# Kernel optimization log

Measured on AMD Instinct MI355X. Metric: run time of the kernel, lower is better.

Reference implementation:

```python
import jax, jax.numpy as jnp
import numpy as np

B, S, E, H = 4, 1024, 1024, 16
HD = E // H  # head_dim = 64


def setup_inputs() -> dict:
    key = jax.random.key(0)
    ks = jax.random.split(key, 7)
    return {
        "query": jax.random.normal(ks[0], (B, S, E), dtype=jnp.float32),
        "key": jax.random.normal(ks[1], (B, S, E), dtype=jnp.float32),
        "value": jax.random.normal(ks[2], (B, S, E), dtype=jnp.float32),
        # per-head Linear weights stacked: [H, head_dim, emb_dim] (torch Linear is y = x @ W^T)
        "Wq": jax.random.normal(ks[3], (H, HD, E), dtype=jnp.float32) * (E ** -0.5),
        "Wk": jax.random.normal(ks[4], (H, HD, E), dtype=jnp.float32) * (E ** -0.5),
        "Wv": jax.random.normal(ks[5], (H, HD, E), dtype=jnp.float32) * (E ** -0.5),
        "Wo": jax.random.normal(ks[6], (E, E), dtype=jnp.float32) * (E ** -0.5),
    }


def reference(query, key, value, Wq, Wk, Wv, Wo):
    # Project per head (all heads vectorized): [B,S,E] x [H,HD,E] -> [B,H,S,HD]
    Q = jnp.einsum('bse,hde->bhsd', query, Wq)
    K = jnp.einsum('bse,hde->bhsd', key, Wk)
    V = jnp.einsum('bse,hde->bhsd', value, Wv)
    scale = 1.0 / np.sqrt(HD)  # source divides by sqrt(emb_dim / n_head)
    scores = jnp.einsum('bhsd,bhtd->bhst', Q, K) * scale  # [B,H,S,S]
    p = jax.nn.softmax(scores, axis=-1)
    ctx = jnp.einsum('bhst,bhtd->bhsd', p, V)  # [B,H,S,HD]
    # concat heads along feature dim -> [B,S,E]
    concat = ctx.transpose(0, 2, 1, 3).reshape(query.shape[0], query.shape[1], -1)
    return concat @ Wo.T
```

## Files before the change

kernel.cpp:

```cpp
#include <hip/hip_runtime.h>

typedef __bf16 bf16_t;
typedef __bf16 bf16x8 __attribute__((ext_vector_type(8)));
typedef float f32x4 __attribute__((ext_vector_type(4)));

#define E_DIM 1024
#define S_LEN 1024
#define NHEAD 16
#define HD_DIM 64
#define BATCH 4
#define TOKENS 4096

__device__ __forceinline__ void async_copy16(const bf16_t* g, bf16_t* l) {
    __builtin_amdgcn_global_load_lds((const __attribute__((address_space(1))) void*)g,
                                     (__attribute__((address_space(3))) void*)l,
                                     16, 0, 0);
}

__global__ __launch_bounds__(256) void cast3(const float* __restrict__ a,
                                             const float* __restrict__ b,
                                             const float* __restrict__ c,
                                             bf16_t* __restrict__ dst, int n) {
    const float* src = blockIdx.y == 0 ? a : (blockIdx.y == 1 ? b : c);
    dst += (size_t)blockIdx.y * n;
    int i = (blockIdx.x * 256 + threadIdx.x) * 8;
    if (i + 8 > n) return;
    float4 x = *(const float4*)(src + i);
    float4 y = *(const float4*)(src + i + 4);
    bf16x8 o;
    o[0] = (bf16_t)x.x; o[1] = (bf16_t)x.y; o[2] = (bf16_t)x.z; o[3] = (bf16_t)x.w;
    o[4] = (bf16_t)y.x; o[5] = (bf16_t)y.y; o[6] = (bf16_t)y.z; o[7] = (bf16_t)y.w;
    *(bf16x8*)(dst + i) = o;
}

__global__ __launch_bounds__(256) void cast4(const float* __restrict__ a,
                                             const float* __restrict__ b,
                                             const float* __restrict__ c,
                                             const float* __restrict__ d,
                                             bf16_t* __restrict__ dst, int n) {
    const float* src = blockIdx.y == 0 ? a : (blockIdx.y == 1 ? b : (blockIdx.y == 2 ? c : d));
    dst += (size_t)blockIdx.y * n;
    int i = (blockIdx.x * 256 + threadIdx.x) * 8;
    if (i + 8 > n) return;
    float4 x = *(const float4*)(src + i);
    float4 y = *(const float4*)(src + i + 4);
    bf16x8 o;
    o[0] = (bf16_t)x.x; o[1] = (bf16_t)x.y; o[2] = (bf16_t)x.z; o[3] = (bf16_t)x.w;
    o[4] = (bf16_t)y.x; o[5] = (bf16_t)y.y; o[6] = (bf16_t)y.z; o[7] = (bf16_t)y.w;
    *(bf16x8*)(dst + i) = o;
}

__global__ __launch_bounds__(256, 4) void proj_gemm(const bf16_t* __restrict__ Xq,
                                                    const bf16_t* __restrict__ Xk,
                                                    const bf16_t* __restrict__ Xv,
                                                    const bf16_t* __restrict__ Wq,
                                                    const bf16_t* __restrict__ Wk,
                                                    const bf16_t* __restrict__ Wv,
                                                    bf16_t* __restrict__ Qp,
                                                    bf16_t* __restrict__ Kp,
                                                    bf16_t* __restrict__ Vp) {
    __shared__ bf16_t sA[128 * 32];
    __shared__ bf16_t sB[128 * 32];
    const int z = blockIdx.z;
    const bf16_t* A = z == 0 ? Xq : (z == 1 ? Xk : Xv);
    const bf16_t* B = z == 0 ? Wq : (z == 1 ? Wk : Wv);
    bf16_t* C = z == 0 ? Qp : (z == 1 ? Kp : Vp);
    const int N = 1024, K = 1024;
    const int lid = blockIdx.x + 8 * blockIdx.y;
    const int m0 = (((lid & 7) << 2) + ((lid >> 3) & 3)) * 128;
    const int n0 = (lid >> 5) * 128;

    const int tid = threadIdx.x;
    const int wave = tid >> 6, lane = tid & 63;
    const int quad = lane >> 4, l16 = lane & 15;
    const int wm = (wave >> 1) * 64, wn = (wave & 1) * 64;
    const int srow = lane >> 2, scol = (lane & 3) * 8;

    f32x4 acc[4][4];
    const f32x4 vzero = {0.f, 0.f, 0.f, 0.f};
#pragma unroll
    for (int mt = 0; mt < 4; mt++)
#pragma unroll
        for (int nt = 0; nt < 4; nt++) acc[mt][nt] = vzero;

    for (int k0 = 0; k0 < K; k0 += 32) {
        __syncthreads();
#pragma unroll
        for (int cc = 0; cc < 4; cc++) {
            int c = wave * 4 + cc;
            const bf16_t* g;
            bf16_t* l;
            if (c < 8) {
                g = A + (size_t)(m0 + c * 16 + srow) * K + k0 + scol;
                l = &sA[c * 16 * 32];
            } else {
                g = B + (size_t)(n0 + (c - 8) * 16 + srow) * K + k0 + scol;
                l = &sB[(c - 8) * 16 * 32];
            }
            async_copy16(g, l);
        }
        asm volatile("s_waitcnt vmcnt(0)" ::: "memory");
        __syncthreads();

        bf16x8 af[4], bfr[4];
#pragma unroll
        for (int mt = 0; mt < 4; mt++)
            af[mt] = *(const bf16x8*)&sA[(wm + mt * 16 + l16) * 32 + quad * 8];
#pragma unroll
        for (int nt = 0; nt < 4; nt++)
            bfr[nt] = *(const bf16x8*)&sB[(wn + nt * 16 + l16) * 32 + quad * 8];
#pragma unroll
        for (int mt = 0; mt < 4; mt++)
#pragma unroll
            for (int nt = 0; nt < 4; nt++)
                acc[mt][nt] = __builtin_amdgcn_mfma_f32_16x16x32_bf16(af[mt], bfr[nt],
                                                                      acc[mt][nt], 0, 0, 0);
    }

#pragma unroll
    for (int mt = 0; mt < 4; mt++)
#pragma unroll
        for (int nt = 0; nt < 4; nt++)
#pragma unroll
            for (int r = 0; r < 4; r++) {
                int row = m0 + wm + mt * 16 + quad * 4 + r;
                int col = n0 + wn + nt * 16 + l16;
                C[(size_t)row * N + col] = (bf16_t)acc[mt][nt][r];
            }
}

#define TM 128
#define TN 64
#define BK 32

template <typename OutT>
__global__ __launch_bounds__(256, 2) void gemm_bt(const bf16_t* __restrict__ A,
                                                  const bf16_t* __restrict__ Bt,
                                                  OutT* __restrict__ C,
                                                  int M, int N, int K) {
    __shared__ bf16_t sA[TM * BK];
    __shared__ bf16_t sB[TN * BK];
    const int tid = threadIdx.x;
    const int wave = tid >> 6, lane = tid & 63;
    const int quad = lane >> 4, l16 = lane & 15;
    const int lid = blockIdx.x + 16 * blockIdx.y;
    const int m0 = (((lid & 7) << 2) + ((lid >> 3) & 3)) * TM;
    const int n0 = (lid >> 5) * TN;
    const int wm = (wave >> 1) * 64;
    const int wn = (wave & 1) * 32;
    const int srow = lane >> 2;
    const int scol = (lane & 3) * 8;

    f32x4 acc[4][2];
    const f32x4 vzero = {0.f, 0.f, 0.f, 0.f};
#pragma unroll
    for (int mt = 0; mt < 4; mt++)
#pragma unroll
        for (int nt = 0; nt < 2; nt++) acc[mt][nt] = vzero;

    for (int k0 = 0; k0 < K; k0 += BK) {
        __syncthreads();
#pragma unroll
        for (int cc = 0; cc < 3; cc++) {
            int c = wave * 3 + cc;
            const bf16_t* g;
            bf16_t* l;
            if (c < 8) {
                g = A + (size_t)(m0 + c * 16 + srow) * K + k0 + scol;
                l = &sA[c * 16 * BK];
            } else {
                g = Bt + (size_t)(n0 + (c - 8) * 16 + srow) * K + k0 + scol;
                l = &sB[(c - 8) * 16 * BK];
            }
            async_copy16(g, l);
        }
        asm volatile("s_waitcnt vmcnt(0)" ::: "memory");
        __syncthreads();

        bf16x8 af[4], bfr[2];
#pragma unroll
        for (int mt = 0; mt < 4; mt++)
            af[mt] = *(const bf16x8*)&sA[(wm + mt * 16 + l16) * BK + quad * 8];
#pragma unroll
        for (int nt = 0; nt < 2; nt++)
            bfr[nt] = *(const bf16x8*)&sB[(wn + nt * 16 + l16) * BK + quad * 8];
#pragma unroll
        for (int mt = 0; mt < 4; mt++)
#pragma unroll
            for (int nt = 0; nt < 2; nt++)
                acc[mt][nt] = __builtin_amdgcn_mfma_f32_16x16x32_bf16(af[mt], bfr[nt],
                                                                      acc[mt][nt], 0, 0, 0);
    }

#pragma unroll
    for (int mt = 0; mt < 4; mt++)
#pragma unroll
        for (int nt = 0; nt < 2; nt++)
#pragma unroll
            for (int r = 0; r < 4; r++) {
                int row = m0 + wm + mt * 16 + quad * 4 + r;
                int col = n0 + wn + nt * 16 + l16;
                C[(size_t)row * N + col] = (OutT)acc[mt][nt][r];
            }
}

#define KPAD 72

__global__ __launch_bounds__(256, 2) void flash_attn(const bf16_t* __restrict__ Q,
                                                     const bf16_t* __restrict__ K,
                                                     const bf16_t* __restrict__ V,
                                                     bf16_t* __restrict__ O) {
    __shared__ bf16_t sK[64 * KPAD];
    __shared__ bf16_t sVt[64 * 64];
    __shared__ bf16_t sP[4 * 32 * KPAD];

    const int tid = threadIdx.x;
    const int wave = tid >> 6, lane = tid & 63;
    const int quad = lane >> 4, l16 = lane & 15;
    const int qt = blockIdx.x, h = blockIdx.y, b = blockIdx.z;
    const size_t base = (size_t)b * S_LEN * E_DIM + h * HD_DIM;
    const float c_exp = 0.125f * 1.44269504089f;

    bf16x8 qf[2][2];
#pragma unroll
    for (int mt = 0; mt < 2; mt++) {
        const bf16_t* qp =
            Q + base + (size_t)(qt * 128 + wave * 32 + mt * 16 + l16) * E_DIM + quad * 8;
        qf[mt][0] = *(const bf16x8*)qp;
        qf[mt][1] = *(const bf16x8*)(qp + 32);
    }

    float lsum[2][4];
    f32x4 accd[2][4];
    const f32x4 vzero = {0.f, 0.f, 0.f, 0.f};
#pragma unroll
    for (int mt = 0; mt < 2; mt++)
#pragma unroll
        for (int r = 0; r < 4; r++) lsum[mt][r] = 0.f;
#pragma unroll
    for (int mt = 0; mt < 2; mt++)
#pragma unroll
        for (int dt = 0; dt < 4; dt++) accd[mt][dt] = vzero;

    const int stg = tid & 7;
    const int ssw = ((stg & 1) << 2) | (stg >> 1);
    int rsw[4];
#pragma unroll
    for (int dt = 0; dt < 4; dt++) {
        int g = dt * 2 + (l16 >> 3);
        rsw[dt] = ((g & 1) << 2) | (g >> 1);
    }
    const int pkey = (l16 >> 2) & 3;
    bf16_t* myP = sP + wave * 32 * KPAD;

    for (int j0 = 0; j0 < S_LEN; j0 += 64) {
        __syncthreads();
#pragma unroll
        for (int it = 0; it < 2; it++) {
            int r = (tid >> 3) + it * 32;
            int c = stg * 8;
            bf16x8 kv = *(const bf16x8*)(K + base + (size_t)(j0 + r) * E_DIM + c);
            *(bf16x8*)&sK[r * KPAD + c] = kv;
            bf16x8 vv = *(const bf16x8*)(V + base + (size_t)(j0 + r) * E_DIM + c);
            int jb = (((r >> 3) ^ ssw) << 3) + (r & 7);
#pragma unroll
            for (int i = 0; i < 8; i++) sVt[(c + i) * 64 + jb] = vv[i];
        }
        __syncthreads();

        bf16x8 kf[4][2];
#pragma unroll
        for (int jt = 0; jt < 4; jt++) {
            kf[jt][0] = *(const bf16x8*)&sK[(jt * 16 + l16) * KPAD + quad * 8];
            kf[jt][1] = *(const bf16x8*)&sK[(jt * 16 + l16) * KPAD + 32 + quad * 8];
        }

#pragma unroll
        for (int mt = 0; mt < 2; mt++) {
            const int prow = mt * 16 + quad * 4;
#pragma unroll
            for (int jt = 0; jt < 4; jt++) {
                f32x4 s = vzero;
                s = __builtin_amdgcn_mfma_f32_16x16x32_bf16(qf[mt][0], kf[jt][0], s, 0, 0, 0);
                s = __builtin_amdgcn_mfma_f32_16x16x32_bf16(qf[mt][1], kf[jt][1], s, 0, 0, 0);
                const int pcol = (((jt * 2 + (l16 >> 3)) ^ quad) << 3) + (l16 & 7);
#pragma unroll
                for (int r = 0; r < 4; r++) {
                    float p = __builtin_amdgcn_exp2f(s[r] * c_exp);
                    lsum[mt][r] += p;
                    myP[(prow + r) * KPAD + pcol] = (bf16_t)p;
                }
            }
        }

        bf16x8 pf[2][2];
#pragma unroll
        for (int mt = 0; mt < 2; mt++)
#pragma unroll
            for (int c = 0; c < 2; c++)
                pf[mt][c] = *(const bf16x8*)&myP[(mt * 16 + l16) * KPAD +
                                                 (((c * 4 + quad) ^ pkey) << 3)];

#pragma unroll
        for (int dt = 0; dt < 4; dt++) {
            bf16x8 vf0 = *(const bf16x8*)&sVt[(dt * 16 + l16) * 64 + ((quad ^ rsw[dt]) << 3)];
            bf16x8 vf1 = *(const bf16x8*)&sVt[(dt * 16 + l16) * 64 + (((4 + quad) ^ rsw[dt]) << 3)];
#pragma unroll
            for (int mt = 0; mt < 2; mt++) {
                accd[mt][dt] = __builtin_amdgcn_mfma_f32_16x16x32_bf16(pf[mt][0], vf0,
                                                                       accd[mt][dt], 0, 0, 0);
                accd[mt][dt] = __builtin_amdgcn_mfma_f32_16x16x32_bf16(pf[mt][1], vf1,
                                                                       accd[mt][dt], 0, 0, 0);
            }
        }
    }

#pragma unroll
    for (int mt = 0; mt < 2; mt++)
#pragma unroll
        for (int r = 0; r < 4; r++) {
#pragma unroll
            for (int m = 1; m < 16; m <<= 1) lsum[mt][r] += __shfl_xor(lsum[mt][r], m);
            float inv = __builtin_amdgcn_rcpf(lsum[mt][r]);
            size_t orow =
                base + (size_t)(qt * 128 + wave * 32 + mt * 16 + quad * 4 + r) * E_DIM;
#pragma unroll
            for (int dt = 0; dt < 4; dt++)
                O[orow + dt * 16 + l16] = (bf16_t)(accd[mt][dt][r] * inv);
        }
}

extern "C" void kernel_launch(void* const* d_in, const int* in_sizes, int n_in,
                              void* d_out, int out_size, void* d_ws, size_t ws_size,
                              hipStream_t stream) {
    const float* q  = (const float*)d_in[0];
    const float* k  = (const float*)d_in[1];
    const float* v  = (const float*)d_in[2];
    const float* wq = (const float*)d_in[3];
    const float* wk = (const float*)d_in[4];
    const float* wv = (const float*)d_in[5];
    const float* wo = (const float*)d_in[6];
    float* out = (float*)d_out;

    const int NX = TOKENS * E_DIM;
    const int NW = E_DIM * E_DIM;

    bf16_t* ws  = (bf16_t*)d_ws;
    bf16_t* Xq  = ws;
    bf16_t* Xk  = ws + (size_t)NX;
    bf16_t* Xv  = ws + (size_t)2 * NX;
    bf16_t* Wqb = ws + (size_t)3 * NX;
    bf16_t* Wkb = Wqb + NW;
    bf16_t* Wvb = Wkb + NW;
    bf16_t* Wob = Wvb + NW;
    bf16_t* Qp  = Wob + NW;
    bf16_t* Kp  = Qp + (size_t)NX;
    bf16_t* Vp  = Kp + (size_t)NX;
    bf16_t* ctx = Xq;

    cast3<<<dim3(NX / 2048, 3), 256, 0, stream>>>(q, k, v, Xq, NX);
    cast4<<<dim3(NW / 2048, 4), 256, 0, stream>>>(wq, wk, wv, wo, Wqb, NW);

    proj_gemm<<<dim3(8, 32, 3), 256, 0, stream>>>(Xq, Xk, Xv, Wqb, Wkb, Wvb, Qp, Kp, Vp);

    flash_attn<<<dim3(S_LEN / 128, NHEAD, BATCH), 256, 0, stream>>>(Qp, Kp, Vp, ctx);

    gemm_bt<float><<<dim3(E_DIM / TN, TOKENS / TM), 256, 0, stream>>>(ctx, Wob, out,
                                                                     TOKENS, E_DIM, E_DIM);
}
```

Before: 204.7 us.

## Keep attention probabilities in registers, merge cast kernels, enlarge output GEMM tile

Flash attention now computes S^T (K as the A operand) so the probabilities come out in a register layout usable directly as the B operand of a 16x16x16 bf16 MFMA. This removes the shared-memory P round-trip and its buffer, and the row sums reduce with two shuffles instead of four. The output is staged through shared memory for vectorized stores, and the grid remaps which heads neighbour each other. The two cast kernels are merged into one launch, and the output projection moves to 128x128 tiles. The trade-offs are twice as many half-width MFMAs for P·V, the transposed-V layout change, and higher register use from the larger GEMM tile.

```diff
diff --git a/kernel.cpp b/kernel.cpp
--- a/kernel.cpp
+++ b/kernel.cpp
@@ -1,8 +1,10 @@
 #include <hip/hip_runtime.h>
 
 typedef __bf16 bf16_t;
+typedef __bf16 bf16x4 __attribute__((ext_vector_type(4)));
 typedef __bf16 bf16x8 __attribute__((ext_vector_type(8)));
 typedef float f32x4 __attribute__((ext_vector_type(4)));
+typedef short short4v __attribute__((ext_vector_type(4)));
 
 #define E_DIM 1024
 #define S_LEN 1024
@@ -17,33 +19,48 @@
                                      16, 0, 0);
 }
 
-__global__ __launch_bounds__(256) void cast3(const float* __restrict__ a,
-                                             const float* __restrict__ b,
-                                             const float* __restrict__ c,
-                                             bf16_t* __restrict__ dst, int n) {
-    const float* src = blockIdx.y == 0 ? a : (blockIdx.y == 1 ? b : c);
-    dst += (size_t)blockIdx.y * n;
-    int i = (blockIdx.x * 256 + threadIdx.x) * 8;
-    if (i + 8 > n) return;
-    float4 x = *(const float4*)(src + i);
-    float4 y = *(const float4*)(src + i + 4);
-    bf16x8 o;
-    o[0] = (bf16_t)x.x; o[1] = (bf16_t)x.y; o[2] = (bf16_t)x.z; o[3] = (bf16_t)x.w;
-    o[4] = (bf16_t)y.x; o[5] = (bf16_t)y.y; o[6] = (bf16_t)y.z; o[7] = (bf16_t)y.w;
-    *(bf16x8*)(dst + i) = o;
-}
-
-__global__ __launch_bounds__(256) void cast4(const float* __restrict__ a,
-                                             const float* __restrict__ b,
-                                             const float* __restrict__ c,
-                                             const float* __restrict__ d,
-                                             bf16_t* __restrict__ dst, int n) {
-    const float* src = blockIdx.y == 0 ? a : (blockIdx.y == 1 ? b : (blockIdx.y == 2 ? c : d));
-    dst += (size_t)blockIdx.y * n;
-    int i = (blockIdx.x * 256 + threadIdx.x) * 8;
-    if (i + 8 > n) return;
-    float4 x = *(const float4*)(src + i);
-    float4 y = *(const float4*)(src + i + 4);
+__device__ __forceinline__ f32x4 pv_mfma(bf16x4 a, bf16x4 b, f32x4 c) {
+#if __has_builtin(__builtin_amdgcn_mfma_f32_16x16x16_bf16)
+    return __builtin_amdgcn_mfma_f32_16x16x16_bf16(a, b, c, 0, 0, 0);
+#elif __has_builtin(__builtin_amdgcn_mfma_f32_16x16x16bf16_1k)
+    short4v as, bs;
+    __builtin_memcpy(&as, &a, 8);
+    __builtin_memcpy(&bs, &b, 8);
+    return __builtin_amdgcn_mfma_f32_16x16x16bf16_1k(as, bs, c, 0, 0, 0);
+#else
+    f32x4 d;
+    asm volatile("v_mfma_f32_16x16x16_bf16 %0, %1, %2, %3\n\ts_nop 7\n\ts_nop 7"
+                 : "=v"(d)
+                 : "v"(a), "v"(b), "v"(c));
+    return d;
+#endif
+}
+
+__global__ __launch_bounds__(256) void cast_all(const float* __restrict__ q,
+                                                const float* __restrict__ k,
+                                                const float* __restrict__ v,
+                                                const float* __restrict__ wq,
+                                                const float* __restrict__ wk,
+                                                const float* __restrict__ wv,
+                                                const float* __restrict__ wo,
+                                                bf16_t* __restrict__ dst) {
+    const size_t NX = (size_t)TOKENS * E_DIM;
+    const size_t NW = (size_t)E_DIM * E_DIM;
+    size_t i = ((size_t)blockIdx.x * 256 + threadIdx.x) * 8;
+    const float* src;
+    size_t off;
+    if (i < 3 * NX) {
+        int a = (int)(i >> 22);
+        src = a == 0 ? q : (a == 1 ? k : v);
+        off = i & (NX - 1);
+    } else {
+        size_t j = i - 3 * NX;
+        int a = (int)(j >> 20);
+        src = a == 0 ? wq : (a == 1 ? wk : (a == 2 ? wv : wo));
+        off = j & (NW - 1);
+    }
+    float4 x = *(const float4*)(src + off);
+    float4 y = *(const float4*)(src + off + 4);
     bf16x8 o;
     o[0] = (bf16_t)x.x; o[1] = (bf16_t)x.y; o[2] = (bf16_t)x.z; o[3] = (bf16_t)x.w;
     o[4] = (bf16_t)y.x; o[5] = (bf16_t)y.y; o[6] = (bf16_t)y.z; o[7] = (bf16_t)y.w;
@@ -129,65 +146,59 @@
             }
 }
 
-#define TM 128
-#define TN 64
-#define BK 32
-
-template <typename OutT>
-__global__ __launch_bounds__(256, 2) void gemm_bt(const bf16_t* __restrict__ A,
-                                                  const bf16_t* __restrict__ Bt,
-                                                  OutT* __restrict__ C,
-                                                  int M, int N, int K) {
-    __shared__ bf16_t sA[TM * BK];
-    __shared__ bf16_t sB[TN * BK];
+__global__ __launch_bounds__(256, 4) void out_gemm(const bf16_t* __restrict__ A,
+                                                   const bf16_t* __restrict__ B,
+                                                   float* __restrict__ C) {
+    __shared__ bf16_t sA[128 * 32];
+    __shared__ bf16_t sB[128 * 32];
+    const int N = 1024, K = 1024;
+    const int lid = blockIdx.x + 8 * blockIdx.y;
+    const int m0 = (((lid & 7) << 2) + ((lid >> 3) & 3)) * 128;
+    const int n0 = (lid >> 5) * 128;
+
     const int tid = threadIdx.x;
     const int wave = tid >> 6, lane = tid & 63;
     const int quad = lane >> 4, l16 = lane & 15;
-    const int lid = blockIdx.x + 16 * blockIdx.y;
-    const int m0 = (((lid & 7) << 2) + ((lid >> 3) & 3)) * TM;
-    const int n0 = (lid >> 5) * TN;
-    const int wm = (wave >> 1) * 64;
-    const int wn = (wave & 1) * 32;
-    const int srow = lane >> 2;
-    const int scol = (lane & 3) * 8;
-
-    f32x4 acc[4][2];
+    const int wm = (wave >> 1) * 64, wn = (wave & 1) * 64;
+    const int srow = lane >> 2, scol = (lane & 3) * 8;
+
+    f32x4 acc[4][4];
     const f32x4 vzero = {0.f, 0.f, 0.f, 0.f};
 #pragma unroll
     for (int mt = 0; mt < 4; mt++)
 #pragma unroll
-        for (int nt = 0; nt < 2; nt++) acc[mt][nt] = vzero;
-
-    for (int k0 = 0; k0 < K; k0 += BK) {
-        __syncthreads();
-#pragma unroll
-        for (int cc = 0; cc < 3; cc++) {
-            int c = wave * 3 + cc;
+        for (int nt = 0; nt < 4; nt++) acc[mt][nt] = vzero;
+
+    for (int k0 = 0; k0 < K; k0 += 32) {
+        __syncthreads();
+#pragma unroll
+        for (int cc = 0; cc < 4; cc++) {
+            int c = wave * 4 + cc;
             const bf16_t* g;
             bf16_t* l;
             if (c < 8) {
                 g = A + (size_t)(m0 + c * 16 + srow) * K + k0 + scol;
-                l = &sA[c * 16 * BK];
+                l = &sA[c * 16 * 32];
             } else {
-                g = Bt + (size_t)(n0 + (c - 8) * 16 + srow) * K + k0 + scol;
-                l = &sB[(c - 8) * 16 * BK];
+                g = B + (size_t)(n0 + (c - 8) * 16 + srow) * K + k0 + scol;
+                l = &sB[(c - 8) * 16 * 32];
             }
             async_copy16(g, l);
         }
         asm volatile("s_waitcnt vmcnt(0)" ::: "memory");
         __syncthreads();
 
-        bf16x8 af[4], bfr[2];
+        bf16x8 af[4], bfr[4];
 #pragma unroll
         for (int mt = 0; mt < 4; mt++)
-            af[mt] = *(const bf16x8*)&sA[(wm + mt * 16 + l16) * BK + quad * 8];
-#pragma unroll
-        for (int nt = 0; nt < 2; nt++)
-            bfr[nt] = *(const bf16x8*)&sB[(wn + nt * 16 + l16) * BK + quad * 8];
+            af[mt] = *(const bf16x8*)&sA[(wm + mt * 16 + l16) * 32 + quad * 8];
+#pragma unroll
+        for (int nt = 0; nt < 4; nt++)
+            bfr[nt] = *(const bf16x8*)&sB[(wn + nt * 16 + l16) * 32 + quad * 8];
 #pragma unroll
         for (int mt = 0; mt < 4; mt++)
 #pragma unroll
-            for (int nt = 0; nt < 2; nt++)
+            for (int nt = 0; nt < 4; nt++)
                 acc[mt][nt] = __builtin_amdgcn_mfma_f32_16x16x32_bf16(af[mt], bfr[nt],
                                                                       acc[mt][nt], 0, 0, 0);
     }
@@ -195,29 +206,31 @@
 #pragma unroll
     for (int mt = 0; mt < 4; mt++)
 #pragma unroll
-        for (int nt = 0; nt < 2; nt++)
+        for (int nt = 0; nt < 4; nt++)
 #pragma unroll
             for (int r = 0; r < 4; r++) {
                 int row = m0 + wm + mt * 16 + quad * 4 + r;
                 int col = n0 + wn + nt * 16 + l16;
-                C[(size_t)row * N + col] = (OutT)acc[mt][nt][r];
-            }
-}
-
-#define KPAD 72
+                C[(size_t)row * N + col] = acc[mt][nt][r];
+            }
+}
+
+#define KP 72
 
 __global__ __launch_bounds__(256, 2) void flash_attn(const bf16_t* __restrict__ Q,
                                                      const bf16_t* __restrict__ K,
                                                      const bf16_t* __restrict__ V,
                                                      bf16_t* __restrict__ O) {
-    __shared__ bf16_t sK[64 * KPAD];
-    __shared__ bf16_t sVt[64 * 64];
-    __shared__ bf16_t sP[4 * 32 * KPAD];
+    __shared__ bf16_t smem[2 * 64 * KP];
+    bf16_t* sK = smem;
+    bf16_t* sVt = smem + 64 * KP;
 
     const int tid = threadIdx.x;
     const int wave = tid >> 6, lane = tid & 63;
     const int quad = lane >> 4, l16 = lane & 15;
-    const int qt = blockIdx.x, h = blockIdx.y, b = blockIdx.z;
+    const int qt = blockIdx.y >> 1;
+    const int h = blockIdx.x * 2 + (blockIdx.y & 1);
+    const int b = blockIdx.z;
     const size_t base = (size_t)b * S_LEN * E_DIM + h * HD_DIM;
     const float c_exp = 0.125f * 1.44269504089f;
 
@@ -230,28 +243,15 @@
         qf[mt][1] = *(const bf16x8*)(qp + 32);
     }
 
-    float lsum[2][4];
-    f32x4 accd[2][4];
+    float lsum[2] = {0.f, 0.f};
+    f32x4 acc[2][4];
     const f32x4 vzero = {0.f, 0.f, 0.f, 0.f};
 #pragma unroll
     for (int mt = 0; mt < 2; mt++)
 #pragma unroll
-        for (int r = 0; r < 4; r++) lsum[mt][r] = 0.f;
-#pragma unroll
-    for (int mt = 0; mt < 2; mt++)
-#pragma unroll
-        for (int dt = 0; dt < 4; dt++) accd[mt][dt] = vzero;
+        for (int dt = 0; dt < 4; dt++) acc[mt][dt] = vzero;
 
     const int stg = tid & 7;
-    const int ssw = ((stg & 1) << 2) | (stg >> 1);
-    int rsw[4];
-#pragma unroll
-    for (int dt = 0; dt < 4; dt++) {
-        int g = dt * 2 + (l16 >> 3);
-        rsw[dt] = ((g & 1) << 2) | (g >> 1);
-    }
-    const int pkey = (l16 >> 2) & 3;
-    bf16_t* myP = sP + wave * 32 * KPAD;
 
     for (int j0 = 0; j0 < S_LEN; j0 += 64) {
         __syncthreads();
@@ -260,73 +260,76 @@
             int r = (tid >> 3) + it * 32;
             int c = stg * 8;
             bf16x8 kv = *(const bf16x8*)(K + base + (size_t)(j0 + r) * E_DIM + c);
-            *(bf16x8*)&sK[r * KPAD + c] = kv;
+            *(bf16x8*)&sK[r * KP + c] = kv;
             bf16x8 vv = *(const bf16x8*)(V + base + (size_t)(j0 + r) * E_DIM + c);
-            int jb = (((r >> 3) ^ ssw) << 3) + (r & 7);
-#pragma unroll
-            for (int i = 0; i < 8; i++) sVt[(c + i) * 64 + jb] = vv[i];
+            int jb = (((r >> 2) ^ stg) << 2) | (r & 3);
+#pragma unroll
+            for (int i = 0; i < 8; i++) sVt[(c + i) * KP + jb] = vv[i];
         }
         __syncthreads();
 
         bf16x8 kf[4][2];
 #pragma unroll
         for (int jt = 0; jt < 4; jt++) {
-            kf[jt][0] = *(const bf16x8*)&sK[(jt * 16 + l16) * KPAD + quad * 8];
-            kf[jt][1] = *(const bf16x8*)&sK[(jt * 16 + l16) * KPAD + 32 + quad * 8];
-        }
-
-#pragma unroll
-        for (int mt = 0; mt < 2; mt++) {
-            const int prow = mt * 16 + quad * 4;
+            kf[jt][0] = *(const bf16x8*)&sK[(jt * 16 + l16) * KP + quad * 8];
+            kf[jt][1] = *(const bf16x8*)&sK[(jt * 16 + l16) * KP + 32 + quad * 8];
+        }
+
+        bf16x4 pb[2][4];
+#pragma unroll
+        for (int mt = 0; mt < 2; mt++)
 #pragma unroll
             for (int jt = 0; jt < 4; jt++) {
                 f32x4 s = vzero;
-                s = __builtin_amdgcn_mfma_f32_16x16x32_bf16(qf[mt][0], kf[jt][0], s, 0, 0, 0);
-                s = __builtin_amdgcn_mfma_f32_16x16x32_bf16(qf[mt][1], kf[jt][1], s, 0, 0, 0);
-                const int pcol = (((jt * 2 + (l16 >> 3)) ^ quad) << 3) + (l16 & 7);
+                s = __builtin_amdgcn_mfma_f32_16x16x32_bf16(kf[jt][0], qf[mt][0], s, 0, 0, 0);
+                s = __builtin_amdgcn_mfma_f32_16x16x32_bf16(kf[jt][1], qf[mt][1], s, 0, 0, 0);
 #pragma unroll
                 for (int r = 0; r < 4; r++) {
                     float p = __builtin_amdgcn_exp2f(s[r] * c_exp);
-                    lsum[mt][r] += p;
-                    myP[(prow + r) * KPAD + pcol] = (bf16_t)p;
+                    lsum[mt] += p;
+                    pb[mt][jt][r] = (bf16_t)p;
                 }
             }
-        }
-
-        bf16x8 pf[2][2];
-#pragma unroll
-        for (int mt = 0; mt < 2; mt++)
-#pragma unroll
-            for (int c = 0; c < 2; c++)
-                pf[mt][c] = *(const bf16x8*)&myP[(mt * 16 + l16) * KPAD +
-                                                 (((c * 4 + quad) ^ pkey) << 3)];
-
-#pragma unroll
-        for (int dt = 0; dt < 4; dt++) {
-            bf16x8 vf0 = *(const bf16x8*)&sVt[(dt * 16 + l16) * 64 + ((quad ^ rsw[dt]) << 3)];
-            bf16x8 vf1 = *(const bf16x8*)&sVt[(dt * 16 + l16) * 64 + (((4 + quad) ^ rsw[dt]) << 3)];
-#pragma unroll
-            for (int mt = 0; mt < 2; mt++) {
-                accd[mt][dt] = __builtin_amdgcn_mfma_f32_16x16x32_bf16(pf[mt][0], vf0,
-                                                                       accd[mt][dt], 0, 0, 0);
-                accd[mt][dt] = __builtin_amdgcn_mfma_f32_16x16x32_bf16(pf[mt][1], vf1,
-                                                                       accd[mt][dt], 0, 0, 0);
-            }
-        }
-    }
-
+
+#pragma unroll
+        for (int jt = 0; jt < 4; jt++)
+#pragma unroll
+            for (int dt = 0; dt < 4; dt++) {
+                int cidx = (jt * 4 + quad) ^ (dt * 2 + (l16 >> 3));
+                bf16x4 vf = *(const bf16x4*)&sVt[(dt * 16 + l16) * KP + cidx * 4];
+#pragma unroll
+                for (int mt = 0; mt < 2; mt++)
+                    acc[mt][dt] = pv_mfma(vf, pb[mt][jt], acc[mt][dt]);
+            }
+    }
+
+    float inv[2];
+#pragma unroll
+    for (int mt = 0; mt < 2; mt++) {
+        lsum[mt] += __shfl_xor(lsum[mt], 16);
+        lsum[mt] += __shfl_xor(lsum[mt], 32);
+        inv[mt] = __builtin_amdgcn_rcpf(lsum[mt]);
+    }
+
+    __syncthreads();
+    bf16_t* ep = smem + wave * 32 * KP;
 #pragma unroll
     for (int mt = 0; mt < 2; mt++)
 #pragma unroll
-        for (int r = 0; r < 4; r++) {
-#pragma unroll
-            for (int m = 1; m < 16; m <<= 1) lsum[mt][r] += __shfl_xor(lsum[mt][r], m);
-            float inv = __builtin_amdgcn_rcpf(lsum[mt][r]);
-            size_t orow =
-                base + (size_t)(qt * 128 + wave * 32 + mt * 16 + quad * 4 + r) * E_DIM;
-#pragma unroll
-            for (int dt = 0; dt < 4; dt++)
-                O[orow + dt * 16 + l16] = (bf16_t)(accd[mt][dt][r] * inv);
+        for (int dt = 0; dt < 4; dt++)
+#pragma unroll
+            for (int r = 0; r < 4; r++)
+                ep[(mt * 16 + l16) * KP + dt * 16 + quad * 4 + r] =
+                    (bf16_t)(acc[mt][dt][r] * inv[mt]);
+#pragma unroll
+    for (int mt = 0; mt < 2; mt++)
+#pragma unroll
+        for (int c = 0; c < 2; c++) {
+            int row = lane >> 2;
+            int col = (lane & 3) * 8 + c * 32;
+            bf16x8 oval = *(const bf16x8*)&ep[(mt * 16 + row) * KP + col];
+            *(bf16x8*)&O[base + (size_t)(qt * 128 + wave * 32 + mt * 16 + row) * E_DIM + col] =
+                oval;
         }
 }
 
@@ -358,13 +361,11 @@
     bf16_t* Vp  = Kp + (size_t)NX;
     bf16_t* ctx = Xq;
 
-    cast3<<<dim3(NX / 2048, 3), 256, 0, stream>>>(q, k, v, Xq, NX);
-    cast4<<<dim3(NW / 2048, 4), 256, 0, stream>>>(wq, wk, wv, wo, Wqb, NW);
+    cast_all<<<8192, 256, 0, stream>>>(q, k, v, wq, wk, wv, wo, Xq);
 
     proj_gemm<<<dim3(8, 32, 3), 256, 0, stream>>>(Xq, Xk, Xv, Wqb, Wkb, Wvb, Qp, Kp, Vp);
 
-    flash_attn<<<dim3(S_LEN / 128, NHEAD, BATCH), 256, 0, stream>>>(Qp, Kp, Vp, ctx);
-
-    gemm_bt<float><<<dim3(E_DIM / TN, TOKENS / TM), 256, 0, stream>>>(ctx, Wob, out,
-                                                                     TOKENS, E_DIM, E_DIM);
-}
+    flash_attn<<<dim3(8, 16, 4), 256, 0, stream>>>(Qp, Kp, Vp, ctx);
+
+    out_gemm<<<dim3(8, 32), 256, 0, stream>>>(ctx, Wob, out);
+}
```

After: 194.7 us. 1.05x faster.
